# Performance work log

Measured on AMD Instinct MI355X. Metric: run time of the kernel, lower is better.

Reference implementation:

```python
import jax, jax.numpy as jnp
import numpy as np

B, C, H, W = 16, 128, 56, 56
QK, HEADS, NWIN, TOPK, MLPR = 128, 4, 7, 4, 3
HD_Q, HD_V = QK // HEADS, C // HEADS
WH, WW = H // NWIN, W // NWIN          # 8, 8 tokens per window side
P2, W2 = NWIN * NWIN, WH * WW          # 49 regions, 64 tokens/region
SCALE = QK ** -0.5                     # BiFormer uses full qk_dim**-0.5 for both router and pixel attn


def _dwconv(x, w, b):
    # x: (B,C,H,W); w: (C,1,k,k) depthwise, odd k with SAME padding == torch padding=k//2
    y = jax.lax.conv_general_dilated(x, w, (1, 1), 'SAME',
                                     feature_group_count=x.shape[1],
                                     dimension_numbers=('NCHW', 'OIHW', 'NCHW'))
    return y + b[None, :, None, None]


def _ln(x, g, b):
    m = x.mean(-1, keepdims=True)
    v = ((x - m) ** 2).mean(-1, keepdims=True)
    return (x - m) * jax.lax.rsqrt(v + 1e-6) * g + b


def _win(t):  # (B,H,W,c) -> (B,P2,WH,WW,c)
    b, _, _, c = t.shape
    return t.reshape(b, NWIN, WH, NWIN, WW, c).transpose(0, 1, 3, 2, 4, 5).reshape(b, P2, WH, WW, c)


def _unwin(t):  # (B,P2,W2,c) -> (B,H,W,c)
    b, c = t.shape[0], t.shape[-1]
    return t.reshape(b, NWIN, NWIN, WH, WW, c).transpose(0, 1, 3, 2, 4, 5).reshape(b, H, W, c)


def setup_inputs() -> dict:
    key = jax.random.key(0)
    ks = jax.random.split(key, 8)
    p = lambda k, sh: (0.02 * jax.random.normal(k, sh)).astype(jnp.float32)
    return {
        'x': jax.random.normal(ks[0], (B, C, H, W), dtype=jnp.float32),
        'pos_w': p(ks[1], (C, 1, 3, 3)), 'pos_b': jnp.zeros((C,), jnp.float32),
        'ln1_g': jnp.ones((C,), jnp.float32), 'ln1_b': jnp.zeros((C,), jnp.float32),
        'qkv_w': p(ks[2], (C, 2 * QK + C)), 'qkv_b': jnp.zeros((2 * QK + C,), jnp.float32),
        'lepe_w': p(ks[3], (C, 1, 5, 5)), 'lepe_b': jnp.zeros((C,), jnp.float32),
        'wo_w': p(ks[4], (C, C)), 'wo_b': jnp.zeros((C,), jnp.float32),
        'ln2_g': jnp.ones((C,), jnp.float32), 'ln2_b': jnp.zeros((C,), jnp.float32),
        'mlp_w1': p(ks[5], (C, MLPR * C)), 'mlp_b1': jnp.zeros((MLPR * C,), jnp.float32),
        'mlp_w2': p(ks[6], (MLPR * C, C)), 'mlp_b2': jnp.zeros((C,), jnp.float32),
    }


def reference(x, pos_w, pos_b, ln1_g, ln1_b, qkv_w, qkv_b, lepe_w, lepe_b,
              wo_w, wo_b, ln2_g, ln2_b, mlp_w1, mlp_b1, mlp_w2, mlp_b2):
    # CPE: x = x + depthwise3x3(x)
    x = x + _dwconv(x, pos_w, pos_b)
    xh = x.transpose(0, 2, 3, 1)                        # NHWC

    # ---- BiLevelRoutingAttention(norm1(x)) ----
    y = _ln(xh, ln1_g, ln1_b)
    qkv = y @ qkv_w + qkv_b                             # (B,H,W,2*QK+C)
    q, kv = qkv[..., :QK], qkv[..., QK:]                # kv = [k | v]
    qw, kvw = _win(q), _win(kv)                         # (B,P2,WH,WW,.)

    # region-level routing: detached window means, coarse affinity, top-k regions
    q_win = jax.lax.stop_gradient(qw.mean((2, 3)))      # (B,P2,QK)
    k_win = jax.lax.stop_gradient(kvw[..., :QK].mean((2, 3)))
    logits = jnp.einsum('bpc,bqc->bpq', q_win * SCALE, k_win)
    _, idx = jax.lax.top_k(logits, TOPK)                # (B,P2,TOPK) int32

    # gather k/v tokens of the selected regions (mul_weight='none': weights unused)
    kv_pix = kvw.reshape(B, P2, W2, QK + C)
    kv_sel = jax.vmap(lambda t, i: t[i])(kv_pix, idx)   # (B,P2,TOPK,W2,QK+C)
    k_sel = kv_sel[..., :QK].reshape(B, P2, TOPK * W2, HEADS, HD_Q)
    v_sel = kv_sel[..., QK:].reshape(B, P2, TOPK * W2, HEADS, HD_V)
    q_pix = qw.reshape(B, P2, W2, HEADS, HD_Q)

    att = jnp.einsum('bpqhd,bpkhd->bphqk', q_pix * SCALE, k_sel)
    att = jax.nn.softmax(att, axis=-1)
    o = jnp.einsum('bphqk,bpkhd->bpqhd', att, v_sel).reshape(B, P2, W2, C)
    o = _unwin(o)                                       # (B,H,W,C)

    # LePE: depthwise 5x5 on v over the full image, then output projection
    v_img = kv[..., QK:].transpose(0, 3, 1, 2)
    lepe = _dwconv(v_img, lepe_w, lepe_b).transpose(0, 2, 3, 1)
    o = (o + lepe) @ wo_w + wo_b
    xh = xh + o

    # ---- MLP(norm2(x)) ----
    z = _ln(xh, ln2_g, ln2_b)
    z = jax.nn.gelu(z @ mlp_w1 + mlp_b1, approximate=False) @ mlp_w2 + mlp_b2
    xh = xh + z
    return xh.transpose(0, 3, 1, 2)                     # back to NCHW
```

## Files before the change

kernel.cpp:

```cpp
#include <hip/hip_runtime.h>
#include <math.h>

#define BATCH 16
#define CH    128
#define HGT   56
#define WID   56
#define NPIX  (BATCH*HGT*WID)
#define NQKV  384
#define NWIN  7
#define P2    49
#define TOPK  4
#define ATT_SCALE 0.088388347648318447f

typedef __attribute__((ext_vector_type(8))) short short8;
typedef __attribute__((ext_vector_type(4))) float float4v;

static __device__ __forceinline__ unsigned short f2bf(float f) {
  unsigned u = __float_as_uint(f);
  u += 0x7fffu + ((u >> 16) & 1u);
  return (unsigned short)(u >> 16);
}
static __device__ __forceinline__ float bf2f(unsigned short u) {
  return __uint_as_float((unsigned)u << 16);
}

__global__ __launch_bounds__(128) void k_prep(
    const float* __restrict__ qkv_w, const float* __restrict__ wo_w,
    const float* __restrict__ mlp_w1, const float* __restrict__ mlp_w2,
    unsigned short* __restrict__ Wq, unsigned short* __restrict__ Wo,
    unsigned short* __restrict__ W1, unsigned short* __restrict__ W2) {
  int bx = blockIdx.x, t = threadIdx.x;
  if (bx < 384) {
    int n = bx;
    Wq[n*128 + t] = f2bf(qkv_w[(size_t)t*384 + n]);
  } else if (bx < 512) {
    int n = bx - 384;
    Wo[n*128 + t] = f2bf(wo_w[(size_t)t*128 + n]);
  } else if (bx < 896) {
    int n = bx - 512;
    W1[n*128 + t] = f2bf(mlp_w1[(size_t)t*384 + n]);
  } else {
    int n = bx - 896;
    for (int k = t; k < 384; k += 128)
      W2[n*384 + k] = f2bf(mlp_w2[(size_t)k*128 + n]);
  }
}

__global__ __launch_bounds__(256) void k_posconv(const float* __restrict__ x,
    const float* __restrict__ pw, const float* __restrict__ pb,
    float* __restrict__ xh) {
  __shared__ float sh[10*58*32];
  int b = blockIdx.y;
  int rg = blockIdx.x >> 2, cg = blockIdx.x & 3;
  int row0 = rg*8, c0 = cg*32;
  int t = threadIdx.x;
  for (int i = t; i < 10*58*32/4; i += 256)
    ((int4*)sh)[i] = make_int4(0,0,0,0);
  __syncthreads();
  for (int i = t; i < 4480; i += 256) {
    int c = i & 31, chunk = (i >> 5) % 14, rr = i / 448;
    int grow = row0 + rr - 1;
    if ((unsigned)grow < HGT) {
      float4 v = *(const float4*)(x + ((size_t)(b*CH + c0 + c))*(HGT*WID)
                                  + grow*WID + chunk*4);
      float* d = &sh[(rr*58 + 1 + chunk*4)*32 + c];
      d[0] = v.x; d[32] = v.y; d[64] = v.z; d[96] = v.w;
    }
  }
  __syncthreads();
  int c = t & 31, pg = t >> 5;
  float w[9];
#pragma unroll
  for (int i = 0; i < 9; i++) w[i] = pw[(c0 + c)*9 + i];
  float bias = pb[c0 + c];
  const float* rowp[3];
#pragma unroll
  for (int dy = 0; dy < 3; dy++) rowp[dy] = &sh[((pg + dy)*58)*32 + c];
  float win[3][3];
#pragma unroll
  for (int j = 0; j < 2; j++)
#pragma unroll
    for (int dy = 0; dy < 3; dy++) win[j][dy] = rowp[dy][j*32];
  float* ob = &xh[(((size_t)b*HGT + row0 + pg)*WID)*CH + c0 + c];
#pragma unroll
  for (int col = 0; col < 56; col++) {
    int slot = (col + 2) % 3;
#pragma unroll
    for (int dy = 0; dy < 3; dy++) win[slot][dy] = rowp[dy][(col + 2)*32];
    float s = bias + win[(col + 1) % 3][1];
#pragma unroll
    for (int dx = 0; dx < 3; dx++) {
      int sl = (col + dx) % 3;
#pragma unroll
      for (int dy = 0; dy < 3; dy++) s += win[sl][dy] * w[dy*3 + dx];
    }
    ob[col*CH] = s;
  }
}

__global__ __launch_bounds__(256, 2) void k_ln_gemm_mfma(
    const float* __restrict__ in, const float* __restrict__ g,
    const float* __restrict__ be, const unsigned short* __restrict__ Wt,
    const float* __restrict__ bias, float* __restrict__ out, int do_gelu) {
  __shared__ __align__(16) unsigned short aL[128*136];
  __shared__ __align__(16) unsigned short bL[128*136];
  size_t base = (size_t)blockIdx.x * 128;
  int t = threadIdx.x;
  {
    int r = t >> 1, half = t & 1;
    const float4* src = (const float4*)(in + (base + r)*CH + half*64);
    float v[64];
    float s = 0.f, ss = 0.f;
#pragma unroll
    for (int i = 0; i < 16; i++) {
      float4 f = src[i];
      v[4*i] = f.x; v[4*i+1] = f.y; v[4*i+2] = f.z; v[4*i+3] = f.w;
      s += f.x + f.y + f.z + f.w;
      ss += f.x*f.x + f.y*f.y + f.z*f.z + f.w*f.w;
    }
    s += __shfl_xor(s, 1); ss += __shfl_xor(ss, 1);
    float m  = s * (1.f/128.f);
    float var = ss * (1.f/128.f) - m*m;
    float rs = rsqrtf(var + 1e-6f);
    union { unsigned short us[8]; int4 v4; } pk;
#pragma unroll
    for (int c8 = 0; c8 < 8; c8++) {
#pragma unroll
      for (int j = 0; j < 8; j++) {
        int ch = half*64 + c8*8 + j;
        pk.us[j] = f2bf((v[c8*8 + j] - m) * rs * g[ch] + be[ch]);
      }
      *(int4*)&aL[r*136 + half*64 + c8*8] = pk.v4;
    }
  }
  int wid = t >> 6, lane = t & 63;
  int ln = lane & 15, q = lane >> 4;
  int wr = (wid >> 1)*64, wc = (wid & 1)*64;
  for (int chunk = 0; chunk < 3; chunk++) {
    if (chunk) __syncthreads();
    for (int i = t; i < 2048; i += 256) {
      int row = i >> 4, seg = i & 15;
      *(int4*)&bL[row*136 + seg*8] =
          *(const int4*)(Wt + (size_t)(chunk*128 + row)*128 + seg*8);
    }
    __syncthreads();
    float4v acc[4][4];
#pragma unroll
    for (int a = 0; a < 4; a++)
#pragma unroll
      for (int b = 0; b < 4; b++)
        acc[a][b] = (float4v){0.f, 0.f, 0.f, 0.f};
#pragma unroll
    for (int kk = 0; kk < 4; kk++) {
      int ko = kk*32 + q*8;
      short8 af[4], bf[4];
#pragma unroll
      for (int mf = 0; mf < 4; mf++)
        af[mf] = *(const short8*)&aL[(wr + mf*16 + ln)*136 + ko];
#pragma unroll
      for (int nf = 0; nf < 4; nf++)
        bf[nf] = *(const short8*)&bL[(wc + nf*16 + ln)*136 + ko];
#pragma unroll
      for (int mf = 0; mf < 4; mf++)
#pragma unroll
        for (int nf = 0; nf < 4; nf++)
          acc[mf][nf] = __builtin_amdgcn_mfma_f32_16x16x32_bf16(
              af[mf], bf[nf], acc[mf][nf], 0, 0, 0);
    }
#pragma unroll
    for (int mf = 0; mf < 4; mf++)
#pragma unroll
      for (int nf = 0; nf < 4; nf++) {
        int row = wr + mf*16 + q*4;
        int col = wc + nf*16 + ln + chunk*128;
        float b4 = bias[col];
#pragma unroll
        for (int j = 0; j < 4; j++) {
          float vv = acc[mf][nf][j] + b4;
          if (do_gelu) vv = 0.5f * vv * (1.f + erff(vv * 0.70710678118654752f));
          out[(base + row + j)*NQKV + col] = vv;
        }
      }
  }
}

__global__ __launch_bounds__(256) void k_pack(const float* __restrict__ qkv,
    unsigned short* __restrict__ vT, unsigned short* __restrict__ qW,
    unsigned short* __restrict__ kW) {
  __shared__ unsigned short tile[128*40];
  int pg0 = blockIdx.x * 32;
  int b = pg0 / (HGT*WID), sp0 = pg0 % (HGT*WID);
  int t = threadIdx.x;
  int pl = t >> 3, seg = t & 7;
  {
    int sp = sp0 + pl;
    int h = sp / WID, w = sp - h*WID;
    int p = (h >> 3)*NWIN + (w >> 3);
    int ploc = (h & 7)*8 + (w & 7);
    const float4* src = (const float4*)(qkv + (size_t)(pg0 + pl)*NQKV + seg*32);
    unsigned short* dst = (seg < 4 ? qW : kW)
        + ((size_t)(b*P2 + p)*64 + ploc)*128 + (seg & 3)*32;
    float sc = (seg < 4) ? ATT_SCALE : 1.f;
    union { unsigned short us[8]; int4 v4; } pk;
#pragma unroll
    for (int g2 = 0; g2 < 4; g2++) {
      float4 f0 = src[g2*2], f1 = src[g2*2 + 1];
      pk.us[0] = f2bf(f0.x*sc); pk.us[1] = f2bf(f0.y*sc);
      pk.us[2] = f2bf(f0.z*sc); pk.us[3] = f2bf(f0.w*sc);
      pk.us[4] = f2bf(f1.x*sc); pk.us[5] = f2bf(f1.y*sc);
      pk.us[6] = f2bf(f1.z*sc); pk.us[7] = f2bf(f1.w*sc);
      *(int4*)&dst[g2*8] = pk.v4;
    }
  }
  {
    const float4* src = (const float4*)(qkv + (size_t)(pg0 + pl)*NQKV + 256 + seg*16);
#pragma unroll
    for (int i = 0; i < 4; i++) {
      float4 f = src[i];
      int c = seg*16 + i*4;
      tile[(c+0)*40 + pl] = f2bf(f.x);
      tile[(c+1)*40 + pl] = f2bf(f.y);
      tile[(c+2)*40 + pl] = f2bf(f.z);
      tile[(c+3)*40 + pl] = f2bf(f.w);
    }
  }
  __syncthreads();
  int c = t >> 1, half = t & 1;
  unsigned short* dst = vT + ((size_t)b*CH + c)*(HGT*WID) + sp0 + half*16;
  const int4* srcl = (const int4*)&tile[c*40 + half*16];
  ((int4*)dst)[0] = srcl[0];
  ((int4*)dst)[1] = srcl[1];
}

__global__ __launch_bounds__(256) void k_winmean(const float* __restrict__ qkv,
    float* __restrict__ qwin, float* __restrict__ kwin) {
  __shared__ float4 red[4][64];
  int bp = blockIdx.x; int b = bp / P2, p = bp % P2;
  int wy = p / NWIN, wx = p % NWIN;
  int w = threadIdx.x >> 6, l = threadIdx.x & 63;
  float4 acc = make_float4(0.f, 0.f, 0.f, 0.f);
#pragma unroll
  for (int i = 0; i < 16; i++) {
    int pix = w*16 + i;
    int ir = pix >> 3, iw = pix & 7;
    size_t po = (((size_t)b*HGT + wy*8 + ir)*WID + wx*8 + iw)*NQKV;
    float4 v = ((const float4*)(qkv + po))[l];
    acc.x += v.x; acc.y += v.y; acc.z += v.z; acc.w += v.w;
  }
  red[w][l] = acc;
  __syncthreads();
  if (w == 0) {
    float4 t0 = red[0][l], t1 = red[1][l], t2 = red[2][l], t3 = red[3][l];
    float4 s = make_float4((t0.x+t1.x+t2.x+t3.x)*(1.f/64.f),
                           (t0.y+t1.y+t2.y+t3.y)*(1.f/64.f),
                           (t0.z+t1.z+t2.z+t3.z)*(1.f/64.f),
                           (t0.w+t1.w+t2.w+t3.w)*(1.f/64.f));
    if (l < 32) ((float4*)(qwin + (size_t)bp*128))[l] = s;
    else        ((float4*)(kwin + (size_t)bp*128))[l - 32] = s;
  }
}

__global__ __launch_bounds__(256) void k_topk(const float* __restrict__ qwin,
    const float* __restrict__ kwin, int* __restrict__ idx) {
  __shared__ float logits[64];
  int bp = blockIdx.x; int b = bp / P2;
  int t = threadIdx.x;
  int key = t >> 2, qu = t & 3;
  float s = 0.f;
  if (key < P2) {
    const float4* qp = (const float4*)(qwin + (size_t)bp*128 + qu*32);
    const float4* kp = (const float4*)(kwin + ((size_t)b*P2 + key)*128 + qu*32);
#pragma unroll
    for (int i = 0; i < 8; i++) {
      float4 qv = qp[i], kv = kp[i];
      s += qv.x*kv.x + qv.y*kv.y + qv.z*kv.z + qv.w*kv.w;
    }
  }
  s += __shfl_xor(s, 1);
  s += __shfl_xor(s, 2);
  if (qu == 0 && key < P2) logits[key] = s;
  __syncthreads();
  if (t == 0) {
    unsigned long long used = 0ULL;
    for (int tt = 0; tt < TOPK; tt++) {
      float best = -1e30f; int bi = 0;
      for (int q = 0; q < P2; q++) {
        bool ok = !((used >> q) & 1ULL);
        float lv = logits[q];
        if (ok && lv > best) { best = lv; bi = q; }
      }
      used |= 1ULL << bi;
      idx[(size_t)bp*TOPK + tt] = bi;
    }
  }
}

#define PLS 72
__global__ __launch_bounds__(256) void k_attn_mfma(
    const unsigned short* __restrict__ qW, const unsigned short* __restrict__ kW,
    const unsigned short* __restrict__ vT, const int* __restrict__ idx,
    float* __restrict__ o) {
  __shared__ unsigned short pL[4][64*PLS];
  int bx = blockIdx.x;
  int b = bx & 15, p = bx >> 4;
  int bp = b*P2 + p;
  int wy = p / NWIN, wx = p % NWIN;
  int h = threadIdx.x >> 6, lane = threadIdx.x & 63;
  int ln = lane & 15, q = lane >> 4;

  short8 aq[4];
#pragma unroll
  for (int mf = 0; mf < 4; mf++)
    aq[mf] = *(const short8*)&qW[((size_t)bp*64 + mf*16 + ln)*128 + h*32 + q*8];

  int4 widx = *(const int4*)&idx[(size_t)bp*TOPK];
  int wins[4] = {widx.x, widx.y, widx.z, widx.w};

  float l_run[4][4];
  float4v facc[4][2];
#pragma unroll
  for (int mf = 0; mf < 4; mf++) {
#pragma unroll
    for (int j = 0; j < 4; j++) l_run[mf][j] = 0.f;
    facc[mf][0] = (float4v){0.f,0.f,0.f,0.f};
    facc[mf][1] = (float4v){0.f,0.f,0.f,0.f};
  }

  unsigned short* myP = &pL[h][0];
  int swr = ((ln >> 2) & 3) * 16;

  for (int r = 0; r < TOPK; r++) {
    int win = wins[r];
    int sy = win / NWIN, sx = win % NWIN;
    short8 bk[4];
#pragma unroll
    for (int nf = 0; nf < 4; nf++)
      bk[nf] = *(const short8*)&kW[(((size_t)b*P2 + win)*64 + nf*16 + ln)*128 + h*32 + q*8];
    float4v sacc[4][4];
#pragma unroll
    for (int mf = 0; mf < 4; mf++)
#pragma unroll
      for (int nf = 0; nf < 4; nf++)
        sacc[mf][nf] = (float4v){0.f,0.f,0.f,0.f};
#pragma unroll
    for (int mf = 0; mf < 4; mf++)
#pragma unroll
      for (int nf = 0; nf < 4; nf++)
        sacc[mf][nf] = __builtin_amdgcn_mfma_f32_16x16x32_bf16(
            aq[mf], bk[nf], sacc[mf][nf], 0, 0, 0);
#pragma unroll
    for (int mf = 0; mf < 4; mf++) {
#pragma unroll
      for (int j = 0; j < 4; j++) {
        float e0 = __expf(sacc[mf][0][j]);
        float e1 = __expf(sacc[mf][1][j]);
        float e2 = __expf(sacc[mf][2][j]);
        float e3 = __expf(sacc[mf][3][j]);
        l_run[mf][j] += (e0 + e1) + (e2 + e3);
        int rowoff = (mf*16 + q*4 + j)*PLS;
        int sww = q*16;
        myP[rowoff + (( 0 + ln) ^ sww)] = f2bf(e0);
        myP[rowoff + ((16 + ln) ^ sww)] = f2bf(e1);
        myP[rowoff + ((32 + ln) ^ sww)] = f2bf(e2);
        myP[rowoff + ((48 + ln) ^ sww)] = f2bf(e3);
      }
    }
#pragma unroll
    for (int kk = 0; kk < 2; kk++) {
      short8 ap[4];
#pragma unroll
      for (int mf = 0; mf < 4; mf++)
        ap[mf] = *(const short8*)&myP[(mf*16 + ln)*PLS + ((kk*32 + q*8) ^ swr)];
      short8 bv[2];
#pragma unroll
      for (int nf2 = 0; nf2 < 2; nf2++) {
        int d = h*32 + nf2*16 + ln;
        int K0 = kk*32 + q*8;
        const unsigned short* vp = vT + ((size_t)b*CH + d)*(HGT*WID)
            + (sy*8 + (K0 >> 3))*WID + sx*8;
        bv[nf2] = *(const short8*)vp;
      }
#pragma unroll
      for (int mf = 0; mf < 4; mf++)
#pragma unroll
        for (int nf2 = 0; nf2 < 2; nf2++)
          facc[mf][nf2] = __builtin_amdgcn_mfma_f32_16x16x32_bf16(
              ap[mf], bv[nf2], facc[mf][nf2], 0, 0, 0);
    }
  }
#pragma unroll
  for (int mf = 0; mf < 4; mf++)
#pragma unroll
    for (int j = 0; j < 4; j++) {
      float l = l_run[mf][j];
      l += __shfl_xor(l, 1);
      l += __shfl_xor(l, 2);
      l += __shfl_xor(l, 4);
      l += __shfl_xor(l, 8);
      float inv = 1.f / l;
      int prow = mf*16 + q*4 + j;
      size_t pg = ((size_t)b*HGT + wy*8 + (prow>>3))*WID + wx*8 + (prow&7);
      o[pg*CH + h*32 + ln]      = facc[mf][0][j] * inv;
      o[pg*CH + h*32 + 16 + ln] = facc[mf][1][j] * inv;
    }
}

__global__ __launch_bounds__(256) void k_lepe(const unsigned short* __restrict__ vT,
    const float* __restrict__ lw, const float* __restrict__ lb,
    float* __restrict__ o) {
  __shared__ unsigned short sh[12*60*32];
  int b = blockIdx.y;
  int rg = blockIdx.x >> 2, cg = blockIdx.x & 3;
  int row0 = rg*8, c0 = cg*32;
  int t = threadIdx.x;
  for (int i = t; i < 12*60*32/8; i += 256)
    ((int4*)sh)[i] = make_int4(0,0,0,0);
  __syncthreads();
  for (int i = t; i < 2688; i += 256) {
    int chunk = i % 7, rr = (i/7) % 12, c = i / 84;
    int grow = row0 + rr - 2;
    if ((unsigned)grow < HGT) {
      int4 v = *(const int4*)(vT + ((size_t)(b*CH + c0 + c))*(HGT*WID) + grow*WID + chunk*8);
      union { int4 v4; unsigned short us[8]; } u; u.v4 = v;
#pragma unroll
      for (int j = 0; j < 8; j++)
        sh[(rr*60 + 2 + chunk*8 + j)*32 + c] = u.us[j];
    }
  }
  __syncthreads();
  int c = t & 31, pg = t >> 5;
  float w[25];
#pragma unroll
  for (int i = 0; i < 25; i++) w[i] = lw[(c0 + c)*25 + i];
  float bias = lb[c0 + c];
  const unsigned short* rowp[5];
#pragma unroll
  for (int dy = 0; dy < 5; dy++) rowp[dy] = &sh[((pg + dy)*60)*32 + c];
  float win[5][5];
#pragma unroll
  for (int j = 0; j < 4; j++)
#pragma unroll
    for (int dy = 0; dy < 5; dy++) win[j][dy] = bf2f(rowp[dy][j*32]);
  float* ob = &o[(((size_t)b*HGT + row0 + pg)*WID)*CH + c0 + c];
#pragma unroll
  for (int col = 0; col < 56; col++) {
    int slot = (col + 4) % 5;
#pragma unroll
    for (int dy = 0; dy < 5; dy++) win[slot][dy] = bf2f(rowp[dy][(col + 4)*32]);
    float s = bias;
#pragma unroll
    for (int dx = 0; dx < 5; dx++) {
      int sl = (col + dx) % 5;
#pragma unroll
      for (int dy = 0; dy < 5; dy++) s += win[sl][dy] * w[dy*5 + dx];
    }
    ob[col*CH] += s;
  }
}

__global__ __launch_bounds__(256, 2) void k_wo_mfma(
    const float* __restrict__ in, const unsigned short* __restrict__ Wt,
    const float* __restrict__ bias, float* __restrict__ xh) {
  __shared__ __align__(16) unsigned short aL[128*136];
  __shared__ __align__(16) unsigned short bL[128*136];
  size_t base = (size_t)blockIdx.x * 128;
  int t = threadIdx.x;
  {
    int r = t >> 1, half = t & 1;
    const float4* src = (const float4*)(in + (base + r)*CH + half*64);
    union { unsigned short us[8]; int4 v4; } pk;
#pragma unroll
    for (int c8 = 0; c8 < 8; c8++) {
      float4 f0 = src[c8*2], f1 = src[c8*2 + 1];
      pk.us[0] = f2bf(f0.x); pk.us[1] = f2bf(f0.y);
      pk.us[2] = f2bf(f0.z); pk.us[3] = f2bf(f0.w);
      pk.us[4] = f2bf(f1.x); pk.us[5] = f2bf(f1.y);
      pk.us[6] = f2bf(f1.z); pk.us[7] = f2bf(f1.w);
      *(int4*)&aL[r*136 + half*64 + c8*8] = pk.v4;
    }
  }
  for (int i = t; i < 2048; i += 256) {
    int row = i >> 4, seg = i & 15;
    *(int4*)&bL[row*136 + seg*8] = *(const int4*)(Wt + (size_t)row*128 + seg*8);
  }
  __syncthreads();
  int wid = t >> 6, lane = t & 63;
  int ln = lane & 15, q = lane >> 4;
  int wr = (wid >> 1)*64, wc = (wid & 1)*64;
  float4v acc[4][4];
#pragma unroll
  for (int a = 0; a < 4; a++)
#pragma unroll
    for (int b = 0; b < 4; b++)
      acc[a][b] = (float4v){0.f, 0.f, 0.f, 0.f};
#pragma unroll
  for (int kk = 0; kk < 4; kk++) {
    int ko = kk*32 + q*8;
    short8 af[4], bf[4];
#pragma unroll
    for (int mf = 0; mf < 4; mf++)
      af[mf] = *(const short8*)&aL[(wr + mf*16 + ln)*136 + ko];
#pragma unroll
    for (int nf = 0; nf < 4; nf++)
      bf[nf] = *(const short8*)&bL[(wc + nf*16 + ln)*136 + ko];
#pragma unroll
    for (int mf = 0; mf < 4; mf++)
#pragma unroll
      for (int nf = 0; nf < 4; nf++)
        acc[mf][nf] = __builtin_amdgcn_mfma_f32_16x16x32_bf16(
            af[mf], bf[nf], acc[mf][nf], 0, 0, 0);
  }
#pragma unroll
  for (int mf = 0; mf < 4; mf++)
#pragma unroll
    for (int nf = 0; nf < 4; nf++) {
      int row = wr + mf*16 + q*4;
      int col = wc + nf*16 + ln;
      float b4 = bias[col];
#pragma unroll
      for (int j = 0; j < 4; j++) {
        float* p = &xh[(base + row + j)*CH + col];
        *p += acc[mf][nf][j] + b4;
      }
    }
}

__global__ __launch_bounds__(256, 2) void k_mlp2_mfma(
    const float* __restrict__ hid, const unsigned short* __restrict__ Wt,
    const float* __restrict__ bias, const float* __restrict__ xh,
    float* __restrict__ out) {
  __shared__ __align__(16) unsigned short aL[128*136];
  __shared__ __align__(16) unsigned short bL[128*136];
  size_t base = (size_t)blockIdx.x * 128;
  int t = threadIdx.x;
  int wid = t >> 6, lane = t & 63;
  int ln = lane & 15, q = lane >> 4;
  int wr = (wid >> 1)*64, wc = (wid & 1)*64;
  float4v acc[4][4];
#pragma unroll
  for (int a = 0; a < 4; a++)
#pragma unroll
    for (int b = 0; b < 4; b++)
      acc[a][b] = (float4v){0.f, 0.f, 0.f, 0.f};
  for (int kc = 0; kc < 3; kc++) {
    if (kc) __syncthreads();
    {
      int r = t >> 1, half = t & 1;
      const float4* src = (const float4*)(hid + (base + r)*NQKV + kc*128 + half*64);
      union { unsigned short us[8]; int4 v4; } pk;
#pragma unroll
      for (int c8 = 0; c8 < 8; c8++) {
        float4 f0 = src[c8*2], f1 = src[c8*2 + 1];
        pk.us[0] = f2bf(f0.x); pk.us[1] = f2bf(f0.y);
        pk.us[2] = f2bf(f0.z); pk.us[3] = f2bf(f0.w);
        pk.us[4] = f2bf(f1.x); pk.us[5] = f2bf(f1.y);
        pk.us[6] = f2bf(f1.z); pk.us[7] = f2bf(f1.w);
        *(int4*)&aL[r*136 + half*64 + c8*8] = pk.v4;
      }
    }
    for (int i = t; i < 2048; i += 256) {
      int row = i >> 4, seg = i & 15;
      *(int4*)&bL[row*136 + seg*8] =
          *(const int4*)(Wt + (size_t)row*NQKV + kc*128 + seg*8);
    }
    __syncthreads();
#pragma unroll
    for (int kk = 0; kk < 4; kk++) {
      int ko = kk*32 + q*8;
      short8 af[4], bf[4];
#pragma unroll
      for (int mf = 0; mf < 4; mf++)
        af[mf] = *(const short8*)&aL[(wr + mf*16 + ln)*136 + ko];
#pragma unroll
      for (int nf = 0; nf < 4; nf++)
        bf[nf] = *(const short8*)&bL[(wc + nf*16 + ln)*136 + ko];
#pragma unroll
      for (int mf = 0; mf < 4; mf++)
#pragma unroll
        for (int nf = 0; nf < 4; nf++)
          acc[mf][nf] = __builtin_amdgcn_mfma_f32_16x16x32_bf16(
              af[mf], bf[nf], acc[mf][nf], 0, 0, 0);
    }
  }
#pragma unroll
  for (int mf = 0; mf < 4; mf++)
#pragma unroll
    for (int nf = 0; nf < 4; nf++) {
      int row = wr + mf*16 + q*4;
      int col = wc + nf*16 + ln;
      float b4 = bias[col];
#pragma unroll
      for (int j = 0; j < 4; j++) {
        size_t pixel = base + row + j;
        int b = (int)(pixel / (HGT*WID));
        int sp = (int)(pixel % (HGT*WID));
        out[((size_t)b*CH + col)*(HGT*WID) + sp] =
            acc[mf][nf][j] + b4 + xh[pixel*CH + col];
      }
    }
}

extern "C" void kernel_launch(void* const* d_in, const int* in_sizes, int n_in,
                              void* d_out, int out_size, void* d_ws, size_t ws_size,
                              hipStream_t stream) {
  const float* x      = (const float*)d_in[0];
  const float* pos_w  = (const float*)d_in[1];
  const float* pos_b  = (const float*)d_in[2];
  const float* ln1_g  = (const float*)d_in[3];
  const float* ln1_b  = (const float*)d_in[4];
  const float* qkv_w  = (const float*)d_in[5];
  const float* qkv_b  = (const float*)d_in[6];
  const float* lepe_w = (const float*)d_in[7];
  const float* lepe_b = (const float*)d_in[8];
  const float* wo_w   = (const float*)d_in[9];
  const float* wo_b   = (const float*)d_in[10];
  const float* ln2_g  = (const float*)d_in[11];
  const float* ln2_b  = (const float*)d_in[12];
  const float* mlp_w1 = (const float*)d_in[13];
  const float* mlp_b1 = (const float*)d_in[14];
  const float* mlp_w2 = (const float*)d_in[15];
  const float* mlp_b2 = (const float*)d_in[16];

  float* ws   = (float*)d_ws;
  float* xh   = ws;
  float* qkv  = xh  + (size_t)NPIX*CH;
  float* o    = qkv + (size_t)NPIX*NQKV;
  float* qwin = o   + (size_t)NPIX*CH;
  float* kwin = qwin + (size_t)BATCH*P2*128;
  int*   idx  = (int*)(kwin + (size_t)BATCH*P2*128);
  unsigned short* Wq = (unsigned short*)(idx + BATCH*P2*TOPK);
  unsigned short* Wo = Wq + 384*128;
  unsigned short* W1 = Wo + 128*128;
  unsigned short* W2 = W1 + 384*128;
  unsigned short* vT = W2 + 128*384;
  unsigned short* qW = vT + (size_t)NPIX*CH;
  unsigned short* kW = qW + (size_t)NPIX*CH;
  float* hid  = qkv;

  k_prep<<<1024, 128, 0, stream>>>(qkv_w, wo_w, mlp_w1, mlp_w2, Wq, Wo, W1, W2);
  k_posconv<<<dim3(28, BATCH), 256, 0, stream>>>(x, pos_w, pos_b, xh);
  k_ln_gemm_mfma<<<NPIX/128, 256, 0, stream>>>(xh, ln1_g, ln1_b, Wq, qkv_b, qkv, 0);
  k_pack<<<NPIX/32, 256, 0, stream>>>(qkv, vT, qW, kW);
  k_winmean<<<BATCH*P2, 256, 0, stream>>>(qkv, qwin, kwin);
  k_topk<<<BATCH*P2, 256, 0, stream>>>(qwin, kwin, idx);
  k_attn_mfma<<<BATCH*P2, 256, 0, stream>>>(qW, kW, vT, idx, o);
  k_lepe<<<dim3(28, BATCH), 256, 0, stream>>>(vT, lepe_w, lepe_b, o);
  k_wo_mfma<<<NPIX/128, 256, 0, stream>>>(o, Wo, wo_b, xh);
  k_ln_gemm_mfma<<<NPIX/128, 256, 0, stream>>>(xh, ln2_g, ln2_b, W1, mlp_b1, hid, 1);
  k_mlp2_mfma<<<NPIX/128, 256, 0, stream>>>(hid, W2, mlp_b2, xh, (float*)d_out);
}
```

Before: 379.9 us.

## Fuse QKV pack into GEMM epilogue, compute router from LN means, store MLP hidden as bf16

The QKV GEMM now writes bf16 windowed q/k and transposed v directly from its epilogue, which removes the fp32 qkv buffer and the separate pack kernel. Routing queries and keys are computed from the per-window mean of the LN1 output times the QKV weights (linear, so mean commutes), replacing the winmean pass over qkv. The MLP hidden activations are stored as bf16 instead of fp32, halving that intermediate's traffic. The risks are scattered 2-byte stores in the q/k epilogue and small rounding differences in the router logits.

New measurement: 327.7 us. -13.8%, faster.

```diff
diff --git a/kernel.cpp b/kernel.cpp
--- a/kernel.cpp
+++ b/kernel.cpp
@@ -13,6 +13,7 @@
 #define ATT_SCALE 0.088388347648318447f
 
 typedef __attribute__((ext_vector_type(8))) short short8;
+typedef __attribute__((ext_vector_type(4))) short short4v;
 typedef __attribute__((ext_vector_type(4))) float float4v;
 
 static __device__ __forceinline__ unsigned short f2bf(float f) {
@@ -98,165 +99,57 @@
   }
 }
 
-__global__ __launch_bounds__(256, 2) void k_ln_gemm_mfma(
-    const float* __restrict__ in, const float* __restrict__ g,
-    const float* __restrict__ be, const unsigned short* __restrict__ Wt,
-    const float* __restrict__ bias, float* __restrict__ out, int do_gelu) {
-  __shared__ __align__(16) unsigned short aL[128*136];
-  __shared__ __align__(16) unsigned short bL[128*136];
-  size_t base = (size_t)blockIdx.x * 128;
+__global__ __launch_bounds__(256) void k_route(const float* __restrict__ xh,
+    const float* __restrict__ g, const float* __restrict__ be,
+    const float* __restrict__ qkv_w, const float* __restrict__ qkv_b,
+    float* __restrict__ qwin, float* __restrict__ kwin) {
+  __shared__ float yt[128*68];
+  __shared__ float ym[128];
+  int bp = blockIdx.x; int b = bp / P2, p = bp % P2;
+  int wy = p / NWIN, wx = p % NWIN;
   int t = threadIdx.x;
+  int pl = t >> 2, qu = t & 3;
   {
-    int r = t >> 1, half = t & 1;
-    const float4* src = (const float4*)(in + (base + r)*CH + half*64);
-    float v[64];
-    float s = 0.f, ss = 0.f;
-#pragma unroll
-    for (int i = 0; i < 16; i++) {
+    int hg = wy*8 + (pl >> 3), wg = wx*8 + (pl & 7);
+    const float4* src = (const float4*)(xh + (((size_t)b*HGT + hg)*WID + wg)*CH + qu*32);
+    float v[32]; float s = 0.f, ss = 0.f;
+#pragma unroll
+    for (int i = 0; i < 8; i++) {
       float4 f = src[i];
       v[4*i] = f.x; v[4*i+1] = f.y; v[4*i+2] = f.z; v[4*i+3] = f.w;
       s += f.x + f.y + f.z + f.w;
       ss += f.x*f.x + f.y*f.y + f.z*f.z + f.w*f.w;
     }
     s += __shfl_xor(s, 1); ss += __shfl_xor(ss, 1);
+    s += __shfl_xor(s, 2); ss += __shfl_xor(ss, 2);
     float m  = s * (1.f/128.f);
     float var = ss * (1.f/128.f) - m*m;
     float rs = rsqrtf(var + 1e-6f);
-    union { unsigned short us[8]; int4 v4; } pk;
-#pragma unroll
-    for (int c8 = 0; c8 < 8; c8++) {
-#pragma unroll
-      for (int j = 0; j < 8; j++) {
-        int ch = half*64 + c8*8 + j;
-        pk.us[j] = f2bf((v[c8*8 + j] - m) * rs * g[ch] + be[ch]);
-      }
-      *(int4*)&aL[r*136 + half*64 + c8*8] = pk.v4;
-    }
-  }
-  int wid = t >> 6, lane = t & 63;
-  int ln = lane & 15, q = lane >> 4;
-  int wr = (wid >> 1)*64, wc = (wid & 1)*64;
-  for (int chunk = 0; chunk < 3; chunk++) {
-    if (chunk) __syncthreads();
-    for (int i = t; i < 2048; i += 256) {
-      int row = i >> 4, seg = i & 15;
-      *(int4*)&bL[row*136 + seg*8] =
-          *(const int4*)(Wt + (size_t)(chunk*128 + row)*128 + seg*8);
-    }
-    __syncthreads();
-    float4v acc[4][4];
-#pragma unroll
-    for (int a = 0; a < 4; a++)
-#pragma unroll
-      for (int b = 0; b < 4; b++)
-        acc[a][b] = (float4v){0.f, 0.f, 0.f, 0.f};
-#pragma unroll
-    for (int kk = 0; kk < 4; kk++) {
-      int ko = kk*32 + q*8;
-      short8 af[4], bf[4];
-#pragma unroll
-      for (int mf = 0; mf < 4; mf++)
-        af[mf] = *(const short8*)&aL[(wr + mf*16 + ln)*136 + ko];
-#pragma unroll
-      for (int nf = 0; nf < 4; nf++)
-        bf[nf] = *(const short8*)&bL[(wc + nf*16 + ln)*136 + ko];
-#pragma unroll
-      for (int mf = 0; mf < 4; mf++)
-#pragma unroll
-        for (int nf = 0; nf < 4; nf++)
-          acc[mf][nf] = __builtin_amdgcn_mfma_f32_16x16x32_bf16(
-              af[mf], bf[nf], acc[mf][nf], 0, 0, 0);
-    }
-#pragma unroll
-    for (int mf = 0; mf < 4; mf++)
-#pragma unroll
-      for (int nf = 0; nf < 4; nf++) {
-        int row = wr + mf*16 + q*4;
-        int col = wc + nf*16 + ln + chunk*128;
-        float b4 = bias[col];
-#pragma unroll
-        for (int j = 0; j < 4; j++) {
-          float vv = acc[mf][nf][j] + b4;
-          if (do_gelu) vv = 0.5f * vv * (1.f + erff(vv * 0.70710678118654752f));
-          out[(base + row + j)*NQKV + col] = vv;
-        }
-      }
-  }
-}
-
-__global__ __launch_bounds__(256) void k_pack(const float* __restrict__ qkv,
-    unsigned short* __restrict__ vT, unsigned short* __restrict__ qW,
-    unsigned short* __restrict__ kW) {
-  __shared__ unsigned short tile[128*40];
-  int pg0 = blockIdx.x * 32;
-  int b = pg0 / (HGT*WID), sp0 = pg0 % (HGT*WID);
-  int t = threadIdx.x;
-  int pl = t >> 3, seg = t & 7;
+#pragma unroll
+    for (int i = 0; i < 32; i++) {
+      int ch = qu*32 + i;
+      yt[ch*68 + pl] = (v[i] - m) * rs * g[ch] + be[ch];
+    }
+  }
+  __syncthreads();
+  if (t < 128) {
+    const float4* col = (const float4*)&yt[t*68];
+    float4 a = make_float4(0.f,0.f,0.f,0.f);
+#pragma unroll
+    for (int i = 0; i < 16; i++) {
+      float4 f = col[i];
+      a.x += f.x; a.y += f.y; a.z += f.z; a.w += f.w;
+    }
+    ym[t] = (a.x + a.y + a.z + a.w) * (1.f/64.f);
+  }
+  __syncthreads();
   {
-    int sp = sp0 + pl;
-    int h = sp / WID, w = sp - h*WID;
-    int p = (h >> 3)*NWIN + (w >> 3);
-    int ploc = (h & 7)*8 + (w & 7);
-    const float4* src = (const float4*)(qkv + (size_t)(pg0 + pl)*NQKV + seg*32);
-    unsigned short* dst = (seg < 4 ? qW : kW)
-        + ((size_t)(b*P2 + p)*64 + ploc)*128 + (seg & 3)*32;
-    float sc = (seg < 4) ? ATT_SCALE : 1.f;
-    union { unsigned short us[8]; int4 v4; } pk;
-#pragma unroll
-    for (int g2 = 0; g2 < 4; g2++) {
-      float4 f0 = src[g2*2], f1 = src[g2*2 + 1];
-      pk.us[0] = f2bf(f0.x*sc); pk.us[1] = f2bf(f0.y*sc);
-      pk.us[2] = f2bf(f0.z*sc); pk.us[3] = f2bf(f0.w*sc);
-      pk.us[4] = f2bf(f1.x*sc); pk.us[5] = f2bf(f1.y*sc);
-      pk.us[6] = f2bf(f1.z*sc); pk.us[7] = f2bf(f1.w*sc);
-      *(int4*)&dst[g2*8] = pk.v4;
-    }
-  }
-  {
-    const float4* src = (const float4*)(qkv + (size_t)(pg0 + pl)*NQKV + 256 + seg*16);
-#pragma unroll
-    for (int i = 0; i < 4; i++) {
-      float4 f = src[i];
-      int c = seg*16 + i*4;
-      tile[(c+0)*40 + pl] = f2bf(f.x);
-      tile[(c+1)*40 + pl] = f2bf(f.y);
-      tile[(c+2)*40 + pl] = f2bf(f.z);
-      tile[(c+3)*40 + pl] = f2bf(f.w);
-    }
-  }
-  __syncthreads();
-  int c = t >> 1, half = t & 1;
-  unsigned short* dst = vT + ((size_t)b*CH + c)*(HGT*WID) + sp0 + half*16;
-  const int4* srcl = (const int4*)&tile[c*40 + half*16];
-  ((int4*)dst)[0] = srcl[0];
-  ((int4*)dst)[1] = srcl[1];
-}
-
-__global__ __launch_bounds__(256) void k_winmean(const float* __restrict__ qkv,
-    float* __restrict__ qwin, float* __restrict__ kwin) {
-  __shared__ float4 red[4][64];
-  int bp = blockIdx.x; int b = bp / P2, p = bp % P2;
-  int wy = p / NWIN, wx = p % NWIN;
-  int w = threadIdx.x >> 6, l = threadIdx.x & 63;
-  float4 acc = make_float4(0.f, 0.f, 0.f, 0.f);
-#pragma unroll
-  for (int i = 0; i < 16; i++) {
-    int pix = w*16 + i;
-    int ir = pix >> 3, iw = pix & 7;
-    size_t po = (((size_t)b*HGT + wy*8 + ir)*WID + wx*8 + iw)*NQKV;
-    float4 v = ((const float4*)(qkv + po))[l];
-    acc.x += v.x; acc.y += v.y; acc.z += v.z; acc.w += v.w;
-  }
-  red[w][l] = acc;
-  __syncthreads();
-  if (w == 0) {
-    float4 t0 = red[0][l], t1 = red[1][l], t2 = red[2][l], t3 = red[3][l];
-    float4 s = make_float4((t0.x+t1.x+t2.x+t3.x)*(1.f/64.f),
-                           (t0.y+t1.y+t2.y+t3.y)*(1.f/64.f),
-                           (t0.z+t1.z+t2.z+t3.z)*(1.f/64.f),
-                           (t0.w+t1.w+t2.w+t3.w)*(1.f/64.f));
-    if (l < 32) ((float4*)(qwin + (size_t)bp*128))[l] = s;
-    else        ((float4*)(kwin + (size_t)bp*128))[l - 32] = s;
+    int n = t;
+    float s = qkv_b[n];
+#pragma unroll 4
+    for (int c = 0; c < 128; c++) s += ym[c] * qkv_w[(size_t)c*NQKV + n];
+    if (n < 128) qwin[(size_t)bp*128 + n] = s;
+    else         kwin[(size_t)bp*128 + n - 128] = s;
   }
 }
 
@@ -291,6 +184,124 @@
       }
       used |= 1ULL << bi;
       idx[(size_t)bp*TOPK + tt] = bi;
+    }
+  }
+}
+
+__global__ __launch_bounds__(256, 2) void k_qkv_gemm(
+    const float* __restrict__ in, const float* __restrict__ g,
+    const float* __restrict__ be, const unsigned short* __restrict__ Wt,
+    const float* __restrict__ bias,
+    unsigned short* __restrict__ qW, unsigned short* __restrict__ kW,
+    unsigned short* __restrict__ vT) {
+  __shared__ __align__(16) unsigned short aL[128*136];
+  __shared__ __align__(16) unsigned short bL[128*136];
+  int base = blockIdx.x * 128;
+  int t = threadIdx.x;
+  {
+    int r = t >> 1, half = t & 1;
+    const float4* src = (const float4*)(in + (size_t)(base + r)*CH + half*64);
+    float v[64];
+    float s = 0.f, ss = 0.f;
+#pragma unroll
+    for (int i = 0; i < 16; i++) {
+      float4 f = src[i];
+      v[4*i] = f.x; v[4*i+1] = f.y; v[4*i+2] = f.z; v[4*i+3] = f.w;
+      s += f.x + f.y + f.z + f.w;
+      ss += f.x*f.x + f.y*f.y + f.z*f.z + f.w*f.w;
+    }
+    s += __shfl_xor(s, 1); ss += __shfl_xor(ss, 1);
+    float m  = s * (1.f/128.f);
+    float var = ss * (1.f/128.f) - m*m;
+    float rs = rsqrtf(var + 1e-6f);
+    union { unsigned short us[8]; int4 v4; } pk;
+#pragma unroll
+    for (int c8 = 0; c8 < 8; c8++) {
+#pragma unroll
+      for (int j = 0; j < 8; j++) {
+        int ch = half*64 + c8*8 + j;
+        pk.us[j] = f2bf((v[c8*8 + j] - m) * rs * g[ch] + be[ch]);
+      }
+      *(int4*)&aL[r*136 + half*64 + c8*8] = pk.v4;
+    }
+  }
+  int wid = t >> 6, lane = t & 63;
+  int ln = lane & 15, q = lane >> 4;
+  int wr = (wid >> 1)*64, wc = (wid & 1)*64;
+  for (int chunk = 0; chunk < 3; chunk++) {
+    if (chunk) __syncthreads();
+    for (int i = t; i < 2048; i += 256) {
+      int row = i >> 4, seg = i & 15;
+      *(int4*)&bL[row*136 + seg*8] =
+          *(const int4*)(Wt + (size_t)(chunk*128 + row)*128 + seg*8);
+    }
+    __syncthreads();
+    float4v acc[4][4];
+#pragma unroll
+    for (int a = 0; a < 4; a++)
+#pragma unroll
+      for (int b2 = 0; b2 < 4; b2++)
+        acc[a][b2] = (float4v){0.f, 0.f, 0.f, 0.f};
+#pragma unroll
+    for (int kk = 0; kk < 4; kk++) {
+      int ko = kk*32 + q*8;
+      short8 af[4], bf[4];
+#pragma unroll
+      for (int mf = 0; mf < 4; mf++)
+        af[mf] = *(const short8*)&aL[(wr + mf*16 + ln)*136 + ko];
+#pragma unroll
+      for (int nf = 0; nf < 4; nf++)
+        bf[nf] = *(const short8*)&bL[(wc + nf*16 + ln)*136 + ko];
+#pragma unroll
+      for (int mf = 0; mf < 4; mf++)
+#pragma unroll
+        for (int nf = 0; nf < 4; nf++)
+          acc[mf][nf] = __builtin_amdgcn_mfma_f32_16x16x32_bf16(
+              af[mf], bf[nf], acc[mf][nf], 0, 0, 0);
+    }
+    if (chunk < 2) {
+      unsigned short* dst = chunk ? kW : qW;
+      float sc = chunk ? 1.f : ATT_SCALE;
+#pragma unroll
+      for (int mf = 0; mf < 4; mf++) {
+#pragma unroll
+        for (int j = 0; j < 4; j++) {
+          int pg = base + wr + mf*16 + q*4 + j;
+          int b  = pg / 3136, sp = pg - b*3136;
+          int hh = sp / 56, ww = sp - hh*56;
+          int p  = (hh >> 3)*NWIN + (ww >> 3);
+          int ploc = (hh & 7)*8 + (ww & 7);
+          size_t rb = ((size_t)(b*P2 + p)*64 + ploc)*128;
+#pragma unroll
+          for (int nf = 0; nf < 4; nf++) {
+            int col = wc + nf*16 + ln;
+            dst[rb + col] = f2bf((acc[mf][nf][j] + bias[chunk*128 + col])*sc);
+          }
+        }
+      }
+    } else {
+      __syncthreads();
+#pragma unroll
+      for (int mf = 0; mf < 4; mf++)
+#pragma unroll
+        for (int nf = 0; nf < 4; nf++) {
+          int row = wr + mf*16 + q*4;
+          int col = wc + nf*16 + ln;
+          float b4 = bias[256 + col];
+          short4v pk;
+#pragma unroll
+          for (int j = 0; j < 4; j++) pk[j] = (short)f2bf(acc[mf][nf][j] + b4);
+          *(short4v*)&bL[col*136 + row] = pk;
+        }
+      __syncthreads();
+      int c = t >> 1, half = t & 1;
+#pragma unroll
+      for (int g8 = 0; g8 < 8; g8++) {
+        int pg0 = base + half*64 + g8*8;
+        int b = pg0 / 3136, sp = pg0 - b*3136;
+        *(int4*)(vT + ((size_t)(b*CH + c))*3136 + sp) =
+            *(int4*)&bL[c*136 + half*64 + g8*8];
+      }
     }
   }
 }
@@ -525,8 +536,94 @@
     }
 }
 
+__global__ __launch_bounds__(256, 2) void k_mlp1_gemm(
+    const float* __restrict__ in, const float* __restrict__ g,
+    const float* __restrict__ be, const unsigned short* __restrict__ Wt,
+    const float* __restrict__ bias, unsigned short* __restrict__ hidb) {
+  __shared__ __align__(16) unsigned short aL[128*136];
+  __shared__ __align__(16) unsigned short bL[128*136];
+  size_t base = (size_t)blockIdx.x * 128;
+  int t = threadIdx.x;
+  {
+    int r = t >> 1, half = t & 1;
+    const float4* src = (const float4*)(in + (base + r)*CH + half*64);
+    float v[64];
+    float s = 0.f, ss = 0.f;
+#pragma unroll
+    for (int i = 0; i < 16; i++) {
+      float4 f = src[i];
+      v[4*i] = f.x; v[4*i+1] = f.y; v[4*i+2] = f.z; v[4*i+3] = f.w;
+      s += f.x + f.y + f.z + f.w;
+      ss += f.x*f.x + f.y*f.y + f.z*f.z + f.w*f.w;
+    }
+    s += __shfl_xor(s, 1); ss += __shfl_xor(ss, 1);
+    float m  = s * (1.f/128.f);
+    float var = ss * (1.f/128.f) - m*m;
+    float rs = rsqrtf(var + 1e-6f);
+    union { unsigned short us[8]; int4 v4; } pk;
+#pragma unroll
+    for (int c8 = 0; c8 < 8; c8++) {
+#pragma unroll
+      for (int j = 0; j < 8; j++) {
+        int ch = half*64 + c8*8 + j;
+        pk.us[j] = f2bf((v[c8*8 + j] - m) * rs * g[ch] + be[ch]);
+      }
+      *(int4*)&aL[r*136 + half*64 + c8*8] = pk.v4;
+    }
+  }
+  int wid = t >> 6, lane = t & 63;
+  int ln = lane & 15, q = lane >> 4;
+  int wr = (wid >> 1)*64, wc = (wid & 1)*64;
+  for (int chunk = 0; chunk < 3; chunk++) {
+    if (chunk) __syncthreads();
+    for (int i = t; i < 2048; i += 256) {
+      int row = i >> 4, seg = i & 15;
+      *(int4*)&bL[row*136 + seg*8] =
+          *(const int4*)(Wt + (size_t)(chunk*128 + row)*128 + seg*8);
+    }
+    __syncthreads();
+    float4v acc[4][4];
+#pragma unroll
+    for (int a = 0; a < 4; a++)
+#pragma unroll
+      for (int b = 0; b < 4; b++)
+        acc[a][b] = (float4v){0.f, 0.f, 0.f, 0.f};
+#pragma unroll
+    for (int kk = 0; kk < 4; kk++) {
+      int ko = kk*32 + q*8;
+      short8 af[4], bf[4];
+#pragma unroll
+      for (int mf = 0; mf < 4; mf++)
+        af[mf] = *(const short8*)&aL[(wr + mf*16 + ln)*136 + ko];
+#pragma unroll
+      for (int nf = 0; nf < 4; nf++)
+        bf[nf] = *(const short8*)&bL[(wc + nf*16 + ln)*136 + ko];
+#pragma unroll
+      for (int mf = 0; mf < 4; mf++)
+#pragma unroll
+        for (int nf = 0; nf < 4; nf++)
+          acc[mf][nf] = __builtin_amdgcn_mfma_f32_16x16x32_bf16(
+              af[mf], bf[nf], acc[mf][nf], 0, 0, 0);
+    }
+#pragma unroll
+    for (int mf = 0; mf < 4; mf++)
+#pragma unroll
+      for (int nf = 0; nf < 4; nf++) {
+        int row = wr + mf*16 + q*4;
+        int col = wc + nf*16 + ln + chunk*128;
+        float b4 = bias[col];
+#pragma unroll
+        for (int j = 0; j < 4; j++) {
+          float vv = acc[mf][nf][j] + b4;
+          vv = 0.5f * vv * (1.f + erff(vv * 0.70710678118654752f));
+          hidb[(base + row + j)*NQKV + col] = f2bf(vv);
+        }
+      }
+  }
+}
+
 __global__ __launch_bounds__(256, 2) void k_mlp2_mfma(
-    const float* __restrict__ hid, const unsigned short* __restrict__ Wt,
+    const unsigned short* __restrict__ hidb, const unsigned short* __restrict__ Wt,
     const float* __restrict__ bias, const float* __restrict__ xh,
     float* __restrict__ out) {
   __shared__ __align__(16) unsigned short aL[128*136];
@@ -546,17 +643,10 @@
     if (kc) __syncthreads();
     {
       int r = t >> 1, half = t & 1;
-      const float4* src = (const float4*)(hid + (base + r)*NQKV + kc*128 + half*64);
-      union { unsigned short us[8]; int4 v4; } pk;
-#pragma unroll
-      for (int c8 = 0; c8 < 8; c8++) {
-        float4 f0 = src[c8*2], f1 = src[c8*2 + 1];
-        pk.us[0] = f2bf(f0.x); pk.us[1] = f2bf(f0.y);
-        pk.us[2] = f2bf(f0.z); pk.us[3] = f2bf(f0.w);
-        pk.us[4] = f2bf(f1.x); pk.us[5] = f2bf(f1.y);
-        pk.us[6] = f2bf(f1.z); pk.us[7] = f2bf(f1.w);
-        *(int4*)&aL[r*136 + half*64 + c8*8] = pk.v4;
-      }
+      const int4* src = (const int4*)(hidb + (base + r)*NQKV + kc*128 + half*64);
+#pragma unroll
+      for (int i = 0; i < 8; i++)
+        *(int4*)&aL[r*136 + half*64 + i*8] = src[i];
     }
     for (int i = t; i < 2048; i += 256) {
       int row = i >> 4, seg = i & 15;
@@ -623,9 +713,8 @@
 
   float* ws   = (float*)d_ws;
   float* xh   = ws;
-  float* qkv  = xh  + (size_t)NPIX*CH;
-  float* o    = qkv + (size_t)NPIX*NQKV;
-  float* qwin = o   + (size_t)NPIX*CH;
+  float* o    = xh + (size_t)NPIX*CH;
+  float* qwin = o  + (size_t)NPIX*CH;
   float* kwin = qwin + (size_t)BATCH*P2*128;
   int*   idx  = (int*)(kwin + (size_t)BATCH*P2*128);
   unsigned short* Wq = (unsigned short*)(idx + BATCH*P2*TOPK);
@@ -635,17 +724,16 @@
   unsigned short* vT = W2 + 128*384;
   unsigned short* qW = vT + (size_t)NPIX*CH;
   unsigned short* kW = qW + (size_t)NPIX*CH;
-  float* hid  = qkv;
+  unsigned short* hidb = kW + (size_t)NPIX*CH;
 
   k_prep<<<1024, 128, 0, stream>>>(qkv_w, wo_w, mlp_w1, mlp_w2, Wq, Wo, W1, W2);
   k_posconv<<<dim3(28, BATCH), 256, 0, stream>>>(x, pos_w, pos_b, xh);
-  k_ln_gemm_mfma<<<NPIX/128, 256, 0, stream>>>(xh, ln1_g, ln1_b, Wq, qkv_b, qkv, 0);
-  k_pack<<<NPIX/32, 256, 0, stream>>>(qkv, vT, qW, kW);
-  k_winmean<<<BATCH*P2, 256, 0, stream>>>(qkv, qwin, kwin);
+  k_route<<<BATCH*P2, 256, 0, stream>>>(xh, ln1_g, ln1_b, qkv_w, qkv_b, qwin, kwin);
   k_topk<<<BATCH*P2, 256, 0, stream>>>(qwin, kwin, idx);
+  k_qkv_gemm<<<NPIX/128, 256, 0, stream>>>(xh, ln1_g, ln1_b, Wq, qkv_b, qW, kW, vT);
   k_attn_mfma<<<BATCH*P2, 256, 0, stream>>>(qW, kW, vT, idx, o);
   k_lepe<<<dim3(28, BATCH), 256, 0, stream>>>(vT, lepe_w, lepe_b, o);
   k_wo_mfma<<<NPIX/128, 256, 0, stream>>>(o, Wo, wo_b, xh);
-  k_ln_gemm_mfma<<<NPIX/128, 256, 0, stream>>>(xh, ln2_g, ln2_b, W1, mlp_b1, hid, 1);
-  k_mlp2_mfma<<<NPIX/128, 256, 0, stream>>>(hid, W2, mlp_b2, xh, (float*)d_out);
-}
+  k_mlp1_gemm<<<NPIX/128, 256, 0, stream>>>(xh, ln2_g, ln2_b, W1, mlp_b1, hidb);
+  k_mlp2_mfma<<<NPIX/128, 256, 0, stream>>>(hidb, W2, mlp_b2, xh, (float*)d_out);
+}
```
